# Optimization experiments

Measured on AMD Instinct MI355X. Metric: run time of the kernel, lower is better.

The kernel has to match this reference:

```python
import jax, jax.numpy as jnp
import numpy as np

B, BS, M, D = 64, 8, 512, 256  # b = bs * neg_sample_num, neg_sample_num = 8
NEG_FILL = -1e10


def setup_inputs() -> dict:
    key = jax.random.key(0)
    ks = jax.random.split(key, 7)
    x = jax.random.normal(ks[0], (B, M, D), jnp.float32)
    y = jax.random.normal(ks[1], (BS, M, D), jnp.float32)
    mask_x = jax.random.randint(ks[2], (B, M), 0, 2).astype(bool).at[:, 0].set(True)
    mask_y = jax.random.randint(ks[3], (BS, M), 0, 2).astype(bool).at[:, 0].set(True)
    scale = 1.0 / np.sqrt(D)
    Wq = jax.random.normal(ks[4], (D, D), jnp.float32) * scale  # torch Linear weight [out,in]
    Wk = jax.random.normal(ks[5], (D, D), jnp.float32) * scale
    Wv = jax.random.normal(ks[6], (D, D), jnp.float32) * scale
    return {"x": x, "y": y, "mask_x": mask_x, "mask_y": mask_y, "Wq": Wq, "Wk": Wk, "Wv": Wv}


def reference(x, y, mask_x, mask_y, Wq, Wk, Wv):
    # Projections (torch Linear: x @ W.T, no bias)
    Qx, Kx, Vx = x @ Wq.T, x @ Wk.T, x @ Wv.T
    Qy, Ky, Vy = y @ Wq.T, y @ Wk.T, y @ Wv.T
    b, m, d = Qx.shape
    bs = Ky.shape[0]
    neg = b // bs  # neg_sample_num branch (bs != b)

    scores_x = jnp.einsum('bid,bjd->bij', Qx, Kx)   # [b,m,m]
    scores_y = jnp.einsum('bid,bjd->bij', Qy, Ky)   # [bs,m,m]
    # Q_x grouped as [bs, neg, m, d] then transposed to [neg, bs, m, d];
    # K_y is tiled over neg (pure broadcast), so contract directly against [bs,m,d].
    Qx_e = Qx.reshape(bs, neg, m, d).swapaxes(0, 1)  # [neg,bs,m,d]
    scores_xy = jnp.einsum('nsid,sjd->nsij', Qx_e, Ky)  # [neg,bs,m,m]

    mx = mask_x[:, :, None]  # [b,m,1]
    my = mask_y[:, :, None]  # [bs,m,1]
    scores_x = jnp.where(mx & mx.swapaxes(1, 2), scores_x, NEG_FILL)
    scores_y = jnp.where(my & my.swapaxes(1, 2), scores_y, NEG_FILL)

    mask_xy = mask_x.reshape(bs, neg, m, 1).swapaxes(0, 1) & mask_y[None, :, None, :]  # [neg,bs,m,m]
    scores_xy = jnp.where(mask_xy, scores_xy, NEG_FILL)

    # y_len[n, s] = sum(mask_y[s]) for every n (repeat/view/sum/transpose in torch)
    y_len = jnp.broadcast_to(jnp.sum(mask_y.astype(jnp.int32), axis=1)[None, :], (neg, bs))

    probs_x = jax.nn.softmax(scores_x, axis=-1)
    probs_y = jax.nn.softmax(scores_y, axis=-1)
    probs_xy = jax.nn.softmax(scores_xy, axis=-1)

    ctx_x = jnp.einsum('bij,bjd->bid', probs_x, Vx)
    ctx_y = jnp.einsum('bij,bjd->bid', probs_y, Vy)
    return (ctx_x, ctx_y, scores_x, scores_y, probs_xy, mask_xy, y_len)
```

## Files before the change

kernel.cpp:

```cpp
#include <hip/hip_runtime.h>
#include <cstdint>

#define NEG_FILL_F (-10000000000.0f)
constexpr int BB     = 64;
constexpr int BS_    = 8;
constexpr int MM     = 512;
constexpr int DD     = 256;
constexpr int ROWS_X = BB * MM;
constexpr int ROWS_Y = BS_ * MM;
constexpr int ROWS_ALL = ROWS_X + ROWS_Y;
constexpr int K3     = 768;

typedef __attribute__((ext_vector_type(8))) short short8;
typedef __attribute__((ext_vector_type(4))) float f32x4;

__device__ inline unsigned short rne_bf16(float f) {
    unsigned int u = __float_as_uint(f);
    u = (u + 0x7FFFu + ((u >> 16) & 1u)) >> 16;
    return (unsigned short)u;
}
__device__ inline float bf2f(unsigned short h) {
    return __uint_as_float(((unsigned int)h) << 16);
}

__device__ inline f32x4 mfma16(short8 a, short8 b, f32x4 c) {
    return __builtin_amdgcn_mfma_f32_16x16x32_bf16(a, b, c, 0, 0, 0);
}

template<int LDW>
__device__ inline void mfma_tiles(const unsigned short (*Ab)[LDW],
                                  const unsigned short (*Bb)[LDW],
                                  int kk, int wrow, int wcol, int lid, int quad,
                                  f32x4 acc[4][4])
{
    short8 af[4], bfr[4];
    #pragma unroll
    for (int i = 0; i < 4; ++i)
        af[i] = *(const short8*)&Ab[wrow + i * 16 + lid][kk + quad * 8];
    #pragma unroll
    for (int j = 0; j < 4; ++j)
        bfr[j] = *(const short8*)&Bb[wcol + j * 16 + lid][kk + quad * 8];
    #pragma unroll
    for (int i = 0; i < 4; ++i)
        #pragma unroll
        for (int j = 0; j < 4; ++j)
            acc[i][j] = mfma16(af[i], bfr[j], acc[i][j]);
}

__device__ inline void stage_768(unsigned short (*dst)[104],
                                 const unsigned short* __restrict__ src,
                                 int ck, int t)
{
    #pragma unroll
    for (int s = 0; s < 6; ++s) {
        const int c   = s * 256 + t;
        const int row = c / 12;
        const int kc  = (c % 12) * 8;
        short8 v = *(const short8*)(src + (size_t)row * K3 + ck * 96 + kc);
        *(short8*)&dst[row][kc] = v;
    }
}

__device__ inline void stage_x96(unsigned short (*dst)[104],
                                 const float* __restrict__ src,
                                 int ck, int t)
{
    #pragma unroll
    for (int s = 0; s < 4; ++s) {
        const int c   = s * 256 + t;
        const int row = c >> 3;
        const int q4  = (c & 7) * 4;
        float4 v = *(const float4*)(src + (size_t)row * DD + ck * 32 + q4);
        const float fv[4] = {v.x, v.y, v.z, v.w};
        unsigned short o[12];
        #pragma unroll
        for (int e = 0; e < 4; ++e) {
            unsigned short h = rne_bf16(fv[e]);
            unsigned short l = rne_bf16(fv[e] - bf2f(h));
            o[e*3+0] = h; o[e*3+1] = l; o[e*3+2] = h;
        }
        ushort4* p = (ushort4*)&dst[row][q4 * 3];
        p[0] = make_ushort4(o[0], o[1], o[2],  o[3]);
        p[1] = make_ushort4(o[4], o[5], o[6],  o[7]);
        p[2] = make_ushort4(o[8], o[9], o[10], o[11]);
    }
}

__global__ __launch_bounds__(256) void convw_kernel(
    const float* __restrict__ Wq, const float* __restrict__ Wk,
    const float* __restrict__ Wv, unsigned short* __restrict__ Wb)
{
    const int g  = blockIdx.x * 256 + threadIdx.x;
    const int e  = g * 8;
    const int zi = e >> 16;
    const int off = e & 65535;
    const float* W = (zi == 0) ? Wq : (zi == 1 ? Wk : Wv);
    float4 v0 = *(const float4*)(W + off);
    float4 v1 = *(const float4*)(W + off + 4);
    const float fv[8] = {v0.x, v0.y, v0.z, v0.w, v1.x, v1.y, v1.z, v1.w};
    unsigned short o[24];
    #pragma unroll
    for (int i = 0; i < 8; ++i) {
        unsigned short h = rne_bf16(fv[i]);
        unsigned short l = rne_bf16(fv[i] - bf2f(h));
        o[i*3+0] = h; o[i*3+1] = h; o[i*3+2] = l;
    }
    unsigned short* dst = Wb + (size_t)zi * 196608 + (size_t)off * 3;
    #pragma unroll
    for (int s = 0; s < 3; ++s) {
        short8 v;
        #pragma unroll
        for (int e2 = 0; e2 < 8; ++e2) v[e2] = (short)o[s*8+e2];
        *(short8*)(dst + s * 8) = v;
    }
}

__global__ __launch_bounds__(256) void proj_kernel(
    const float* __restrict__ x, const float* __restrict__ y,
    const unsigned short* __restrict__ Wb,
    unsigned short* __restrict__ Qa, unsigned short* __restrict__ Kb,
    unsigned short* __restrict__ Vt)
{
    const int z    = blockIdx.z;
    const int row0 = blockIdx.x * 128;
    const int col0 = blockIdx.y * 128;
    const float* A = (row0 < ROWS_X) ? (x + (size_t)row0 * DD)
                                     : (y + (size_t)(row0 - ROWS_X) * DD);
    const unsigned short* Bsrc = Wb + (size_t)z * 196608 + (size_t)col0 * K3;

    __shared__ unsigned short Ab[128][104];
    __shared__ unsigned short Bb[128][104];

    const int t = threadIdx.x;
    const int wave = t >> 6, lane = t & 63, quad = lane >> 4, lid = lane & 15;
    const int wrow = (wave & 1) * 64, wcol = (wave >> 1) * 64;

    f32x4 acc[4][4];
    #pragma unroll
    for (int i = 0; i < 4; ++i)
        #pragma unroll
        for (int j = 0; j < 4; ++j) acc[i][j] = (f32x4){0.f, 0.f, 0.f, 0.f};

    for (int ck = 0; ck < 8; ++ck) {
        stage_x96(Ab, A, ck, t);
        stage_768(Bb, Bsrc, ck, t);
        __syncthreads();
        #pragma unroll
        for (int kk = 0; kk < 96; kk += 32)
            mfma_tiles<104>(Ab, Bb, kk, wrow, wcol, lid, quad, acc);
        __syncthreads();
    }

    if (z == 2) {
        #pragma unroll
        for (int i = 0; i < 4; ++i) {
            const int rg = row0 + wrow + i * 16 + quad * 4;
            const int b  = rg >> 9;
            const int j  = rg & 511;
            #pragma unroll
            for (int jt = 0; jt < 4; ++jt) {
                const int col = col0 + wcol + jt * 16 + lid;
                *(ushort4*)(Vt + (size_t)b * DD * MM + (size_t)col * MM + j) =
                    make_ushort4(rne_bf16(acc[i][jt][0]), rne_bf16(acc[i][jt][1]),
                                 rne_bf16(acc[i][jt][2]), rne_bf16(acc[i][jt][3]));
            }
        }
    } else {
        unsigned short* dst = (z == 0) ? Qa : Kb;
        const bool aform = (z == 0);
        #pragma unroll
        for (int i = 0; i < 4; ++i) {
            const int rg = row0 + wrow + i * 16 + quad * 4;
            #pragma unroll
            for (int r = 0; r < 4; ++r) {
                unsigned short* rowp = dst + (size_t)(rg + r) * K3;
                #pragma unroll
                for (int jt = 0; jt < 4; ++jt) {
                    const int col = col0 + wcol + jt * 16 + lid;
                    const float v = acc[i][jt][r];
                    unsigned short h = rne_bf16(v);
                    unsigned short l = rne_bf16(v - bf2f(h));
                    rowp[3*col+0] = h;
                    rowp[3*col+1] = aform ? l : h;
                    rowp[3*col+2] = aform ? h : l;
                }
            }
        }
    }
}

__global__ __launch_bounds__(256) void scores_kernel(
    const unsigned short* __restrict__ Qa_base,
    const unsigned short* __restrict__ Kb_base,
    const int* __restrict__ mq_base, const int* __restrict__ mk_base,
    float* __restrict__ Sbase, float* __restrict__ Mbase, int mode)
{
    const int z = blockIdx.z;
    int bq, bk;
    if (mode == 2) { const int n = z >> 3, s = z & 7; bq = s * 8 + n; bk = s; }
    else           { bq = z; bk = z; }

    const int row0 = blockIdx.x * 128;
    const int col0 = blockIdx.y * 128;
    const unsigned short* Asrc = Qa_base + (size_t)(bq * MM + row0) * K3;
    const unsigned short* Bsrc = Kb_base + (size_t)(bk * MM + col0) * K3;
    const int* mq = mq_base + bq * MM;
    const int* mk = mk_base + bk * MM;
    float* S  = Sbase + (size_t)z * MM * MM;
    float* Mo = (mode == 2) ? (Mbase + (size_t)z * MM * MM) : nullptr;

    __shared__ unsigned short Ab[128][104];
    __shared__ unsigned short Bb[128][104];

    const int t = threadIdx.x;
    const int wave = t >> 6, lane = t & 63, quad = lane >> 4, lid = lane & 15;
    const int wrow = (wave & 1) * 64, wcol = (wave >> 1) * 64;

    f32x4 acc[4][4];
    #pragma unroll
    for (int i = 0; i < 4; ++i)
        #pragma unroll
        for (int j = 0; j < 4; ++j) acc[i][j] = (f32x4){0.f, 0.f, 0.f, 0.f};

    for (int ck = 0; ck < 8; ++ck) {
        stage_768(Ab, Asrc, ck, t);
        stage_768(Bb, Bsrc, ck, t);
        __syncthreads();
        #pragma unroll
        for (int kk = 0; kk < 96; kk += 32)
            mfma_tiles<104>(Ab, Bb, kk, wrow, wcol, lid, quad, acc);
        __syncthreads();
    }

    int mcol[4];
    #pragma unroll
    for (int jt = 0; jt < 4; ++jt) mcol[jt] = mk[col0 + wcol + jt * 16 + lid];

    #pragma unroll
    for (int i = 0; i < 4; ++i) {
        const int rg = row0 + wrow + i * 16 + quad * 4;
        #pragma unroll
        for (int r = 0; r < 4; ++r) {
            const bool mr = (mq[rg + r] != 0);
            float* Srow = S + (size_t)(rg + r) * MM;
            float* Mrow = Mo ? (Mo + (size_t)(rg + r) * MM) : nullptr;
            #pragma unroll
            for (int jt = 0; jt < 4; ++jt) {
                const int col = col0 + wcol + jt * 16 + lid;
                const bool valid = mr && (mcol[jt] != 0);
                Srow[col] = valid ? acc[i][jt][r] : NEG_FILL_F;
                if (Mrow) Mrow[col] = valid ? 1.0f : 0.0f;
            }
        }
    }
}

__global__ __launch_bounds__(256) void stats_kernel(
    const float* __restrict__ S, float2* __restrict__ st)
{
    const int wid  = threadIdx.x >> 6;
    const int lane = threadIdx.x & 63;
    const int row  = blockIdx.x * 4 + wid;
    const float* r = S + (size_t)row * MM;

    float4 v0 = *(const float4*)(r + lane * 8);
    float4 v1 = *(const float4*)(r + lane * 8 + 4);

    float m = fmaxf(fmaxf(fmaxf(v0.x, v0.y), fmaxf(v0.z, v0.w)),
                    fmaxf(fmaxf(v1.x, v1.y), fmaxf(v1.z, v1.w)));
    #pragma unroll
    for (int off = 32; off; off >>= 1) m = fmaxf(m, __shfl_xor(m, off));

    float s = __expf(v0.x - m) + __expf(v0.y - m) + __expf(v0.z - m) + __expf(v0.w - m)
            + __expf(v1.x - m) + __expf(v1.y - m) + __expf(v1.z - m) + __expf(v1.w - m);
    #pragma unroll
    for (int off = 32; off; off >>= 1) s += __shfl_xor(s, off);

    if (lane == 0) st[row] = make_float2(m, 1.0f / s);
}

__global__ __launch_bounds__(256) void ctx_kernel(
    const float* __restrict__ Sbase, const float2* __restrict__ stats,
    const unsigned short* __restrict__ Vt_base, float* __restrict__ Obase)
{
    const int b = blockIdx.z;
    const float*          S  = Sbase + (size_t)b * MM * MM;
    const float2*         st = stats + (size_t)b * MM;
    const unsigned short* Vt = Vt_base + (size_t)b * DD * MM;
    float*                O  = Obase + (size_t)b * MM * DD;

    const int row0 = blockIdx.x * 128;
    const int col0 = blockIdx.y * 128;

    __shared__ unsigned short Ab[128][72];
    __shared__ unsigned short Bb[128][72];

    const int t = threadIdx.x;
    const int wave = t >> 6, lane = t & 63, quad = lane >> 4, lid = lane & 15;
    const int wrow = (wave & 1) * 64, wcol = (wave >> 1) * 64;

    f32x4 acc[4][4];
    #pragma unroll
    for (int i = 0; i < 4; ++i)
        #pragma unroll
        for (int j = 0; j < 4; ++j) acc[i][j] = (f32x4){0.f, 0.f, 0.f, 0.f};

    for (int ck = 0; ck < 8; ++ck) {
        #pragma unroll
        for (int s = 0; s < 4; ++s) {
            const int c   = s * 256 + t;
            const int row = c >> 3;
            const int j8  = (c & 7) * 8;
            const float* sp = S + (size_t)(row0 + row) * MM + ck * 64 + j8;
            float4 v0 = *(const float4*)sp;
            float4 v1 = *(const float4*)(sp + 4);
            const float pm = st[row0 + row].x;
            short8 pk;
            pk[0] = (short)rne_bf16(__expf(v0.x - pm));
            pk[1] = (short)rne_bf16(__expf(v0.y - pm));
            pk[2] = (short)rne_bf16(__expf(v0.z - pm));
            pk[3] = (short)rne_bf16(__expf(v0.w - pm));
            pk[4] = (short)rne_bf16(__expf(v1.x - pm));
            pk[5] = (short)rne_bf16(__expf(v1.y - pm));
            pk[6] = (short)rne_bf16(__expf(v1.z - pm));
            pk[7] = (short)rne_bf16(__expf(v1.w - pm));
            *(short8*)&Ab[row][j8] = pk;
            *(short8*)&Bb[row][j8] =
                *(const short8*)(Vt + (size_t)(col0 + row) * MM + ck * 64 + j8);
        }
        __syncthreads();
        #pragma unroll
        for (int kk = 0; kk < 64; kk += 32)
            mfma_tiles<72>(Ab, Bb, kk, wrow, wcol, lid, quad, acc);
        __syncthreads();
    }

    #pragma unroll
    for (int i = 0; i < 4; ++i) {
        const int rgb = row0 + wrow + i * 16 + quad * 4;
        float inv[4];
        #pragma unroll
        for (int r = 0; r < 4; ++r) inv[r] = st[rgb + r].y;
        #pragma unroll
        for (int jt = 0; jt < 4; ++jt) {
            const int col = col0 + wcol + jt * 16 + lid;
            #pragma unroll
            for (int r = 0; r < 4; ++r)
                O[(size_t)(rgb + r) * DD + col] = acc[i][jt][r] * inv[r];
        }
    }
}

__global__ __launch_bounds__(128) void softmax_apply(
    float* __restrict__ S, const float2* __restrict__ stats)
{
    const int row = blockIdx.x;
    const float2 st = stats[row];
    float4* r = (float4*)(S + (size_t)row * MM) + threadIdx.x;
    float4 v = *r;
    v.x = __expf(v.x - st.x) * st.y;
    v.y = __expf(v.y - st.x) * st.y;
    v.z = __expf(v.z - st.x) * st.y;
    v.w = __expf(v.w - st.x) * st.y;
    *r = v;
}

__global__ void ylen_kernel(const int* __restrict__ mask_y, float* __restrict__ out)
{
    const int t = threadIdx.x;
    const int s = t & 7;
    int c = 0;
    for (int i = 0; i < MM; ++i) c += (mask_y[s * MM + i] != 0);
    out[t] = (float)c;
}

extern "C" void kernel_launch(void* const* d_in, const int* in_sizes, int n_in,
                              void* d_out, int out_size, void* d_ws, size_t ws_size,
                              hipStream_t stream)
{
    const float* x      = (const float*)d_in[0];
    const float* y      = (const float*)d_in[1];
    const int*   mask_x = (const int*)d_in[2];
    const int*   mask_y = (const int*)d_in[3];
    const float* Wq     = (const float*)d_in[4];
    const float* Wk     = (const float*)d_in[5];
    const float* Wv     = (const float*)d_in[6];
    float* out = (float*)d_out;

    unsigned short* Wb = (unsigned short*)d_ws;
    unsigned short* Qa = Wb + 589824;
    unsigned short* Kb = Qa + 28311552;
    unsigned short* Vt = Kb + 28311552;
    float2* stats_x  = (float2*)(Vt + 9437184);
    float2* stats_y  = stats_x + ROWS_X;
    float2* stats_xy = stats_y + ROWS_Y;

    float* out_ctx_x = out;
    float* out_ctx_y = out + 8388608;
    float* out_sx    = out + 9437184;
    float* out_sy    = out + 26214400;
    float* out_pxy   = out + 28311552;
    float* out_mxy   = out + 45088768;
    float* out_ylen  = out + 61865984;

    convw_kernel<<<96, 256, 0, stream>>>(Wq, Wk, Wv, Wb);

    proj_kernel<<<dim3(288, 2, 3), 256, 0, stream>>>(x, y, Wb, Qa, Kb, Vt);

    const unsigned short* Qa_y = Qa + (size_t)ROWS_X * K3;
    const unsigned short* Kb_y = Kb + (size_t)ROWS_X * K3;

    scores_kernel<<<dim3(4, 4, 64), 256, 0, stream>>>(Qa,   Kb,   mask_x, mask_x, out_sx,  nullptr, 0);
    scores_kernel<<<dim3(4, 4, 8),  256, 0, stream>>>(Qa_y, Kb_y, mask_y, mask_y, out_sy,  nullptr, 1);
    scores_kernel<<<dim3(4, 4, 64), 256, 0, stream>>>(Qa,   Kb_y, mask_x, mask_y, out_pxy, out_mxy, 2);

    stats_kernel<<<ROWS_X / 4, 256, 0, stream>>>(out_sx,  stats_x);
    stats_kernel<<<ROWS_Y / 4, 256, 0, stream>>>(out_sy,  stats_y);
    stats_kernel<<<ROWS_X / 4, 256, 0, stream>>>(out_pxy, stats_xy);

    ctx_kernel<<<dim3(4, 2, 64), 256, 0, stream>>>(out_sx, stats_x, Vt, out_ctx_x);
    ctx_kernel<<<dim3(4, 2, 8),  256, 0, stream>>>(out_sy, stats_y,
                                                   Vt + (size_t)64 * DD * MM, out_ctx_y);

    softmax_apply<<<ROWS_X, 128, 0, stream>>>(out_pxy, stats_xy);

    ylen_kernel<<<1, 64, 0, stream>>>(mask_y, out_ylen);
}
```

Before: 568.7 us.

## Fuse softmax row stats into scores epilogue and use async global-to-LDS loads

The scores kernel now computes per-tile row max and sum-exp partials in its epilogue, and a small reduce kernel merges the four column-tile partials. This replaces the stats kernels that re-read the full score matrices. The GEMM staging in the proj, scores and ctx kernels moves to global_load_lds direct-to-LDS copies with unpadded LDS rows, which removes the register round trip. The unpadded rows may cause LDS bank conflicts on the MFMA fragment reads. The ylen kernel is also parallelised.

```diff
diff --git a/kernel.cpp b/kernel.cpp
--- a/kernel.cpp
+++ b/kernel.cpp
@@ -27,9 +27,15 @@
     return __builtin_amdgcn_mfma_f32_16x16x32_bf16(a, b, c, 0, 0, 0);
 }
 
-template<int LDW>
-__device__ inline void mfma_tiles(const unsigned short (*Ab)[LDW],
-                                  const unsigned short (*Bb)[LDW],
+__device__ inline void gld16(const unsigned short* g, unsigned short* l) {
+    __builtin_amdgcn_global_load_lds(
+        (const __attribute__((address_space(1))) unsigned int*)g,
+        (__attribute__((address_space(3))) unsigned int*)l, 16, 0, 0);
+}
+
+template<int LDA, int LDB>
+__device__ inline void mfma_tiles(const unsigned short (*Ab)[LDA],
+                                  const unsigned short (*Bb)[LDB],
                                   int kk, int wrow, int wcol, int lid, int quad,
                                   f32x4 acc[4][4])
 {
@@ -47,21 +53,21 @@
             acc[i][j] = mfma16(af[i], bfr[j], acc[i][j]);
 }
 
-__device__ inline void stage_768(unsigned short (*dst)[104],
-                                 const unsigned short* __restrict__ src,
-                                 int ck, int t)
+__device__ inline void stage768_async(unsigned short* dstbase,
+                                      const unsigned short* __restrict__ src,
+                                      int ck, int wave, int lane)
 {
     #pragma unroll
     for (int s = 0; s < 6; ++s) {
-        const int c   = s * 256 + t;
+        const int c   = s * 256 + wave * 64 + lane;
         const int row = c / 12;
         const int kc  = (c % 12) * 8;
-        short8 v = *(const short8*)(src + (size_t)row * K3 + ck * 96 + kc);
-        *(short8*)&dst[row][kc] = v;
-    }
-}
-
-__device__ inline void stage_x96(unsigned short (*dst)[104],
+        gld16(src + (size_t)row * K3 + ck * 96 + kc,
+              dstbase + (size_t)(s * 256 + wave * 64) * 8);
+    }
+}
+
+__device__ inline void stage_x96(unsigned short (*dst)[96],
                                  const float* __restrict__ src,
                                  int ck, int t)
 {
@@ -128,8 +134,8 @@
                                      : (y + (size_t)(row0 - ROWS_X) * DD);
     const unsigned short* Bsrc = Wb + (size_t)z * 196608 + (size_t)col0 * K3;
 
-    __shared__ unsigned short Ab[128][104];
-    __shared__ unsigned short Bb[128][104];
+    __shared__ unsigned short Ab[128][96];
+    __shared__ unsigned short Bb[128][96];
 
     const int t = threadIdx.x;
     const int wave = t >> 6, lane = t & 63, quad = lane >> 4, lid = lane & 15;
@@ -142,12 +148,12 @@
         for (int j = 0; j < 4; ++j) acc[i][j] = (f32x4){0.f, 0.f, 0.f, 0.f};
 
     for (int ck = 0; ck < 8; ++ck) {
+        stage768_async(&Bb[0][0], Bsrc, ck, wave, lane);
         stage_x96(Ab, A, ck, t);
-        stage_768(Bb, Bsrc, ck, t);
         __syncthreads();
         #pragma unroll
         for (int kk = 0; kk < 96; kk += 32)
-            mfma_tiles<104>(Ab, Bb, kk, wrow, wcol, lid, quad, acc);
+            mfma_tiles<96,96>(Ab, Bb, kk, wrow, wcol, lid, quad, acc);
         __syncthreads();
     }
 
@@ -193,7 +199,8 @@
     const unsigned short* __restrict__ Qa_base,
     const unsigned short* __restrict__ Kb_base,
     const int* __restrict__ mq_base, const int* __restrict__ mk_base,
-    float* __restrict__ Sbase, float* __restrict__ Mbase, int mode)
+    float* __restrict__ Sbase, float* __restrict__ Mbase,
+    float2* __restrict__ pstats, int mode)
 {
     const int z = blockIdx.z;
     int bq, bk;
@@ -209,8 +216,10 @@
     float* S  = Sbase + (size_t)z * MM * MM;
     float* Mo = (mode == 2) ? (Mbase + (size_t)z * MM * MM) : nullptr;
 
-    __shared__ unsigned short Ab[128][104];
-    __shared__ unsigned short Bb[128][104];
+    __shared__ unsigned short Ab[128][96];
+    __shared__ unsigned short Bb[128][96];
+    __shared__ float pm2[128][2];
+    __shared__ float ps2[128][2];
 
     const int t = threadIdx.x;
     const int wave = t >> 6, lane = t & 63, quad = lane >> 4, lid = lane & 15;
@@ -223,12 +232,12 @@
         for (int j = 0; j < 4; ++j) acc[i][j] = (f32x4){0.f, 0.f, 0.f, 0.f};
 
     for (int ck = 0; ck < 8; ++ck) {
-        stage_768(Ab, Asrc, ck, t);
-        stage_768(Bb, Bsrc, ck, t);
+        stage768_async(&Ab[0][0], Asrc, ck, wave, lane);
+        stage768_async(&Bb[0][0], Bsrc, ck, wave, lane);
         __syncthreads();
         #pragma unroll
         for (int kk = 0; kk < 96; kk += 32)
-            mfma_tiles<104>(Ab, Bb, kk, wrow, wcol, lid, quad, acc);
+            mfma_tiles<96,96>(Ab, Bb, kk, wrow, wcol, lid, quad, acc);
         __syncthreads();
     }
 
@@ -238,45 +247,58 @@
 
     #pragma unroll
     for (int i = 0; i < 4; ++i) {
-        const int rg = row0 + wrow + i * 16 + quad * 4;
+        const int rl0 = wrow + i * 16 + quad * 4;
         #pragma unroll
         for (int r = 0; r < 4; ++r) {
-            const bool mr = (mq[rg + r] != 0);
-            float* Srow = S + (size_t)(rg + r) * MM;
-            float* Mrow = Mo ? (Mo + (size_t)(rg + r) * MM) : nullptr;
+            const int rlocal = rl0 + r;
+            const int rg = row0 + rlocal;
+            const bool mr = (mq[rg] != 0);
+            float* Srow = S + (size_t)rg * MM;
+            float* Mrow = Mo ? (Mo + (size_t)rg * MM) : nullptr;
+            float v[4];
+            float mt = -3.4e38f;
             #pragma unroll
             for (int jt = 0; jt < 4; ++jt) {
                 const int col = col0 + wcol + jt * 16 + lid;
                 const bool valid = mr && (mcol[jt] != 0);
-                Srow[col] = valid ? acc[i][jt][r] : NEG_FILL_F;
+                v[jt] = valid ? acc[i][jt][r] : NEG_FILL_F;
+                Srow[col] = v[jt];
                 if (Mrow) Mrow[col] = valid ? 1.0f : 0.0f;
+                mt = fmaxf(mt, v[jt]);
             }
-        }
-    }
-}
-
-__global__ __launch_bounds__(256) void stats_kernel(
-    const float* __restrict__ S, float2* __restrict__ st)
-{
-    const int wid  = threadIdx.x >> 6;
-    const int lane = threadIdx.x & 63;
-    const int row  = blockIdx.x * 4 + wid;
-    const float* r = S + (size_t)row * MM;
-
-    float4 v0 = *(const float4*)(r + lane * 8);
-    float4 v1 = *(const float4*)(r + lane * 8 + 4);
-
-    float m = fmaxf(fmaxf(fmaxf(v0.x, v0.y), fmaxf(v0.z, v0.w)),
-                    fmaxf(fmaxf(v1.x, v1.y), fmaxf(v1.z, v1.w)));
-    #pragma unroll
-    for (int off = 32; off; off >>= 1) m = fmaxf(m, __shfl_xor(m, off));
-
-    float s = __expf(v0.x - m) + __expf(v0.y - m) + __expf(v0.z - m) + __expf(v0.w - m)
-            + __expf(v1.x - m) + __expf(v1.y - m) + __expf(v1.z - m) + __expf(v1.w - m);
-    #pragma unroll
-    for (int off = 32; off; off >>= 1) s += __shfl_xor(s, off);
-
-    if (lane == 0) st[row] = make_float2(m, 1.0f / s);
+            #pragma unroll
+            for (int o = 1; o < 16; o <<= 1) mt = fmaxf(mt, __shfl_xor(mt, o));
+            float se = 0.f;
+            #pragma unroll
+            for (int jt = 0; jt < 4; ++jt) se += __expf(v[jt] - mt);
+            #pragma unroll
+            for (int o = 1; o < 16; o <<= 1) se += __shfl_xor(se, o);
+            if (lid == 0) { pm2[rlocal][wave >> 1] = mt; ps2[rlocal][wave >> 1] = se; }
+        }
+    }
+    __syncthreads();
+    if (t < 128) {
+        const float m0 = pm2[t][0], m1 = pm2[t][1];
+        const float mm = fmaxf(m0, m1);
+        const float ss = ps2[t][0] * __expf(m0 - mm) + ps2[t][1] * __expf(m1 - mm);
+        pstats[(size_t)(z * 4 + blockIdx.y) * MM + row0 + t] = make_float2(mm, ss);
+    }
+}
+
+__global__ __launch_bounds__(256) void reduce4_kernel(
+    const float2* __restrict__ p, float2* __restrict__ st)
+{
+    const int row = blockIdx.x * 256 + threadIdx.x;
+    const int z = row >> 9, rl = row & 511;
+    float m = -3.4e38f, s = 0.f;
+    #pragma unroll
+    for (int by = 0; by < 4; ++by) {
+        float2 v = p[(size_t)(z * 4 + by) * MM + rl];
+        float nm = fmaxf(m, v.x);
+        s = s * __expf(m - nm) + v.y * __expf(v.x - nm);
+        m = nm;
+    }
+    st[row] = make_float2(m, 1.0f / s);
 }
 
 __global__ __launch_bounds__(256) void ctx_kernel(
@@ -293,7 +315,7 @@
     const int col0 = blockIdx.y * 128;
 
     __shared__ unsigned short Ab[128][72];
-    __shared__ unsigned short Bb[128][72];
+    __shared__ unsigned short Bb[128][64];
 
     const int t = threadIdx.x;
     const int wave = t >> 6, lane = t & 63, quad = lane >> 4, lid = lane & 15;
@@ -306,6 +328,14 @@
         for (int j = 0; j < 4; ++j) acc[i][j] = (f32x4){0.f, 0.f, 0.f, 0.f};
 
     for (int ck = 0; ck < 8; ++ck) {
+        #pragma unroll
+        for (int s = 0; s < 4; ++s) {
+            const int c   = s * 256 + wave * 64 + lane;
+            const int row = c >> 3;
+            const int j8  = (c & 7) * 8;
+            gld16(Vt + (size_t)(col0 + row) * MM + ck * 64 + j8,
+                  &Bb[0][0] + (size_t)(s * 256 + wave * 64) * 8);
+        }
         #pragma unroll
         for (int s = 0; s < 4; ++s) {
             const int c   = s * 256 + t;
@@ -325,13 +355,11 @@
             pk[6] = (short)rne_bf16(__expf(v1.z - pm));
             pk[7] = (short)rne_bf16(__expf(v1.w - pm));
             *(short8*)&Ab[row][j8] = pk;
-            *(short8*)&Bb[row][j8] =
-                *(const short8*)(Vt + (size_t)(col0 + row) * MM + ck * 64 + j8);
         }
         __syncthreads();
         #pragma unroll
         for (int kk = 0; kk < 64; kk += 32)
-            mfma_tiles<72>(Ab, Bb, kk, wrow, wcol, lid, quad, acc);
+            mfma_tiles<72,64>(Ab, Bb, kk, wrow, wcol, lid, quad, acc);
         __syncthreads();
     }
 
@@ -367,11 +395,14 @@
 
 __global__ void ylen_kernel(const int* __restrict__ mask_y, float* __restrict__ out)
 {
-    const int t = threadIdx.x;
-    const int s = t & 7;
+    const int s = blockIdx.x;
+    const int lane = threadIdx.x;
     int c = 0;
-    for (int i = 0; i < MM; ++i) c += (mask_y[s * MM + i] != 0);
-    out[t] = (float)c;
+    #pragma unroll
+    for (int k = 0; k < 8; ++k) c += (mask_y[s * MM + k * 64 + lane] != 0);
+    #pragma unroll
+    for (int off = 32; off; off >>= 1) c += __shfl_xor(c, off);
+    if (lane < 8) out[lane * 8 + s] = (float)c;
 }
 
 extern "C" void kernel_launch(void* const* d_in, const int* in_sizes, int n_in,
@@ -394,6 +425,9 @@
     float2* stats_x  = (float2*)(Vt + 9437184);
     float2* stats_y  = stats_x + ROWS_X;
     float2* stats_xy = stats_y + ROWS_Y;
+    float2* ps_x  = stats_xy + ROWS_X;
+    float2* ps_y  = ps_x + 64 * 4 * 512;
+    float2* ps_xy = ps_y + 8 * 4 * 512;
 
     float* out_ctx_x = out;
     float* out_ctx_y = out + 8388608;
@@ -410,13 +444,13 @@
     const unsigned short* Qa_y = Qa + (size_t)ROWS_X * K3;
     const unsigned short* Kb_y = Kb + (size_t)ROWS_X * K3;
 
-    scores_kernel<<<dim3(4, 4, 64), 256, 0, stream>>>(Qa,   Kb,   mask_x, mask_x, out_sx,  nullptr, 0);
-    scores_kernel<<<dim3(4, 4, 8),  256, 0, stream>>>(Qa_y, Kb_y, mask_y, mask_y, out_sy,  nullptr, 1);
-    scores_kernel<<<dim3(4, 4, 64), 256, 0, stream>>>(Qa,   Kb_y, mask_x, mask_y, out_pxy, out_mxy, 2);
-
-    stats_kernel<<<ROWS_X / 4, 256, 0, stream>>>(out_sx,  stats_x);
-    stats_kernel<<<ROWS_Y / 4, 256, 0, stream>>>(out_sy,  stats_y);
-    stats_kernel<<<ROWS_X / 4, 256, 0, stream>>>(out_pxy, stats_xy);
+    scores_kernel<<<dim3(4, 4, 64), 256, 0, stream>>>(Qa,   Kb,   mask_x, mask_x, out_sx,  nullptr, ps_x,  0);
+    scores_kernel<<<dim3(4, 4, 8),  256, 0, stream>>>(Qa_y, Kb_y, mask_y, mask_y, out_sy,  nullptr, ps_y,  1);
+    scores_kernel<<<dim3(4, 4, 64), 256, 0, stream>>>(Qa,   Kb_y, mask_x, mask_y, out_pxy, out_mxy, ps_xy, 2);
+
+    reduce4_kernel<<<ROWS_X / 256, 256, 0, stream>>>(ps_x,  stats_x);
+    reduce4_kernel<<<ROWS_Y / 256, 256, 0, stream>>>(ps_y,  stats_y);
+    reduce4_kernel<<<ROWS_X / 256, 256, 0, stream>>>(ps_xy, stats_xy);
 
     ctx_kernel<<<dim3(4, 2, 64), 256, 0, stream>>>(out_sx, stats_x, Vt, out_ctx_x);
     ctx_kernel<<<dim3(4, 2, 8),  256, 0, stream>>>(out_sy, stats_y,
@@ -424,5 +458,5 @@
 
     softmax_apply<<<ROWS_X, 128, 0, stream>>>(out_pxy, stats_xy);
 
-    ylen_kernel<<<1, 64, 0, stream>>>(mask_y, out_ylen);
-}
+    ylen_kernel<<<8, 64, 0, stream>>>(mask_y, out_ylen);
+}
```

Measured after the change: 550.4 us. 1.03x faster.
